# Performance work log

Hardware: AMD Instinct MI355X
Metric: run time of the kernel (lower is better)

The kernel has to match this reference:

```python
import jax, jax.numpy as jnp
import numpy as np

N_FLUID = 16384
N_BND = 2048
SUPPORT = float(np.sqrt(16.0 / (np.pi * N_FLUID)))  # ~16 neighbors avg
NB = 8  # basis functions per axis (n = m = 8)
NM = NB * NB
LAYERS = [32, 64, 64, 2]
F_IN = 8
B_IN = 8


def _radius(queries, points, r):
    """numpy brute-force (chunked) radius search; rows = query idx, cols = point idx."""
    r2 = np.float32(r * r)
    pn = (points ** 2).sum(-1)
    qi_all, pj_all = [], []
    for s in range(0, queries.shape[0], 4096):
        q = queries[s:s + 4096]
        d2 = (q ** 2).sum(-1)[:, None] + pn[None, :] - 2.0 * (q @ points.T)
        qi, pj = np.nonzero(d2 < r2)
        qi_all.append(qi + s)
        pj_all.append(pj)
    return (np.concatenate(qi_all).astype(np.int32),
            np.concatenate(pj_all).astype(np.int32))


def setup_inputs() -> dict:
    rng = np.random.default_rng(0)
    fluid_pos = rng.random((N_FLUID, 2)).astype(np.float32)
    # boundary particles along the perimeter of the unit square
    t = np.linspace(0.0, 4.0, N_BND, endpoint=False).astype(np.float32)
    side = np.floor(t).astype(np.int64)
    frac = t - side
    bx = np.where(side == 0, frac, np.where(side == 1, 1.0, np.where(side == 2, 1.0 - frac, 0.0)))
    by = np.where(side == 0, 0.0, np.where(side == 1, frac, np.where(side == 2, 1.0, 1.0 - frac)))
    bnd_pos = np.stack([bx, by], -1).astype(np.float32)

    # fluid-fluid radius graph (centerIgnore: drop self edges)
    fi, fj = _radius(fluid_pos, fluid_pos, SUPPORT)
    keep = fi != fj
    f_tgt, f_src = fi[keep], fj[keep]
    # fluid(query) - boundary(source) radius graph
    b_tgt, b_src = _radius(fluid_pos, bnd_pos, SUPPORT)

    def conv_w(k, cin, cout):
        return (0.05 * rng.standard_normal((NM, cin, cout))).astype(np.float32)

    def lin_w(cin, cout):
        s = np.sqrt(6.0 / (cin + cout))
        return rng.uniform(-s, s, (cin, cout)).astype(np.float32)

    d = {
        'fluid_pos': jnp.asarray(fluid_pos),
        'bnd_pos': jnp.asarray(bnd_pos),
        'fluid_feat': jnp.asarray(rng.standard_normal((N_FLUID, F_IN)).astype(np.float32)),
        'bnd_feat': jnp.asarray(rng.standard_normal((N_BND, B_IN)).astype(np.float32)),
        'f_tgt': jnp.asarray(f_tgt), 'f_src': jnp.asarray(f_src),
        'b_tgt': jnp.asarray(b_tgt), 'b_src': jnp.asarray(b_src),
        # convs: c0 fluid->fluid (F_IN->32), c1 boundary->fluid (B_IN->32),
        #        c2 (96->64), c3 (64->64), c4 (64->2)
        'Wc0': jnp.asarray(conv_w(0, F_IN, 32)), 'bc0': jnp.zeros((32,), jnp.float32),
        'Wc1': jnp.asarray(conv_w(1, B_IN, 32)), 'bc1': jnp.zeros((32,), jnp.float32),
        'Wc2': jnp.asarray(conv_w(2, 96, 64)), 'bc2': jnp.zeros((64,), jnp.float32),
        'Wc3': jnp.asarray(conv_w(3, 64, 64)), 'bc3': jnp.zeros((64,), jnp.float32),
        'Wc4': jnp.asarray(conv_w(4, 64, 2)), 'bc4': jnp.zeros((2,), jnp.float32),
        # dense branch: l0 (F_IN->32), l1 (96->64), l2 (64->64), l3 (64->2)
        'Wl0': jnp.asarray(lin_w(F_IN, 32)), 'bl0': jnp.zeros((32,), jnp.float32),
        'Wl1': jnp.asarray(lin_w(96, 64)), 'bl1': jnp.zeros((64,), jnp.float32),
        'Wl2': jnp.asarray(lin_w(64, 64)), 'bl2': jnp.zeros((64,), jnp.float32),
        'Wl3': jnp.asarray(lin_w(64, 2)), 'bl3': jnp.zeros((2,), jnp.float32),
    }
    return d


def _hat(x, n):
    # linear 'hat' RBF basis on centers in [-1, 1]
    c = jnp.linspace(-1.0, 1.0, n, dtype=x.dtype)
    return jnp.maximum(0.0, 1.0 - jnp.abs(x[:, None] - c[None, :]) * ((n - 1) / 2.0))


def _polar(d):
    # polar coordinate mapping of normalized displacement d in [-1,1]^2
    r = jnp.sqrt(jnp.sum(d * d, -1) + 1e-12)
    theta = jnp.arctan2(d[:, 1], d[:, 0])
    return jnp.clip(jnp.stack([2.0 * r - 1.0, theta / jnp.pi], -1), -1.0, 1.0)


def _rbf_conv(x_src_nodes, src, tgt, disp, W, b, num_tgt):
    m = _polar(disp)                                   # [E,2]
    bx = _hat(m[:, 0], NB)                             # [E,n]
    by = _hat(m[:, 1], NB)                             # [E,m]
    basis = (bx[:, :, None] * by[:, None, :]).reshape(-1, NM)  # [E,nm]
    xs = x_src_nodes[src]                              # [E,cin]
    acc0 = jnp.zeros((xs.shape[0], W.shape[-1]), xs.dtype)

    def body(acc, wb):
        Wk, bk = wb
        return acc + bk[:, None] * (xs @ Wk), None

    msg, _ = jax.lax.scan(body, acc0, (W, basis.T))    # sum_k basis_k * (xs @ W_k)
    return jax.ops.segment_sum(msg, tgt, num_segments=num_tgt) + b


def reference(fluid_pos, bnd_pos, fluid_feat, bnd_feat, f_tgt, f_src, b_tgt, b_src,
              Wc0, bc0, Wc1, bc1, Wc2, bc2, Wc3, bc3, Wc4, bc4,
              Wl0, bl0, Wl1, bl1, Wl2, bl2, Wl3, bl3):
    N = fluid_feat.shape[0]
    fdisp = jnp.clip(-(fluid_pos[f_src] - fluid_pos[f_tgt]) / SUPPORT, -1.0, 1.0)
    bdisp = jnp.clip((bnd_pos[b_src] - fluid_pos[b_tgt]) / SUPPORT, -1.0, 1.0)

    lin = fluid_feat @ Wl0 + bl0
    fconv = _rbf_conv(fluid_feat, f_src, f_tgt, fdisp, Wc0, bc0, N)
    bconv = _rbf_conv(bnd_feat, b_src, b_tgt, bdisp, Wc1, bc1, N)
    ans = jnp.concatenate([lin, fconv, bconv], axis=-1)  # [N, 96]

    blocks = [(Wc2, bc2, Wl1, bl1, False), (Wc3, bc3, Wl2, bl2, True), (Wc4, bc4, Wl3, bl3, False)]
    for Wc, bc, Wl, bl, residual in blocks:
        a = jax.nn.relu(ans)
        c = _rbf_conv(a, f_src, f_tgt, fdisp, Wc, bc, N)
        dns = a @ Wl + bl
        ans = c + dns + ans if residual else c + dns
    return ans / 128.0
```

## Files before the change

### kernel.cpp

```cpp
#include <hip/hip_runtime.h>
#include <math.h>
#include <stdint.h>

#define NFL   16384
#define NCC   55
#define PADQ  256

struct EdgeData { int src; int ixiy; float fx; float fy; };

typedef _Float16 half8 __attribute__((ext_vector_type(8)));
typedef __attribute__((ext_vector_type(4))) float f32x4;

__device__ __forceinline__ float frelu(float x){ return x > 0.f ? x : 0.f; }
__device__ __forceinline__ unsigned short f2bf(float f){
    unsigned int u = __float_as_uint(f);
    unsigned int r = (u + 0x7FFFu + ((u >> 16) & 1u)) >> 16;
    return (unsigned short)r;
}

__device__ __forceinline__ EdgeData make_edge(const float* qpos, const float* ppos,
                                              int t, int s, float support, float sgn)
{
    float dx = sgn * (ppos[2*s]   - qpos[2*t])   / support;
    float dy = sgn * (ppos[2*s+1] - qpos[2*t+1]) / support;
    dx = fminf(1.f, fmaxf(-1.f, dx));
    dy = fminf(1.f, fmaxf(-1.f, dy));
    float r  = sqrtf(dx*dx + dy*dy + 1e-12f);
    float th = atan2f(dy, dx);
    float m0 = fminf(1.f, fmaxf(-1.f, 2.f*r - 1.f));
    float m1 = fminf(1.f, fmaxf(-1.f, th * 0.3183098861837907f));
    float u = (m0 + 1.f) * 3.5f;
    float v = (m1 + 1.f) * 3.5f;
    int ix = (int)u; if (ix > 6) ix = 6;
    int iy = (int)v; if (iy > 6) iy = 6;
    EdgeData ed;
    ed.src  = s;
    ed.ixiy = ix*8 + iy;
    ed.fx   = u - (float)ix;
    ed.fy   = v - (float)iy;
    return ed;
}

__global__ __launch_bounds__(256)
void setup_k(const float* __restrict__ fluid_pos, const float* __restrict__ bnd_pos,
             const int* __restrict__ f_tgt, const int* __restrict__ f_src, int nEf,
             const int* __restrict__ b_tgt, const int* __restrict__ b_src, int nEb,
             float support,
             EdgeData* __restrict__ edF, EdgeData* __restrict__ edB,
             int* __restrict__ cnt,
             int* __restrict__ rowptrF, int* __restrict__ rowptrB,
             const float* __restrict__ Wc2, const float* __restrict__ Wc3,
             const float* __restrict__ Wc0,
             _Float16* __restrict__ wt2, _Float16* __restrict__ wt3,
             unsigned short* __restrict__ wb0,
             int nA, int nB, int nC)
{
    __shared__ int lc[64];
    __shared__ _Float16 T[64][98];
    int b = blockIdx.x, tid = threadIdx.x;
    if (b < nA){
        if (tid < 64) lc[tid] = 0;
        __syncthreads();
        int e = b*256 + tid;
        if (e < nEf){
            EdgeData d = make_edge(fluid_pos, fluid_pos, f_tgt[e], f_src[e], support, -1.f);
            edF[e] = d;
            atomicAdd(&lc[d.ixiy], 1);
        }
        __syncthreads();
        if (tid < 64 && lc[tid] > 0) atomicAdd(&cnt[tid], lc[tid]);
    } else if (b < nA + nB){
        int e = (b - nA)*256 + tid;
        if (e < nEb)
            edB[e] = make_edge(fluid_pos, bnd_pos, b_tgt[e], b_src[e], support, 1.f);
    } else if (b < nA + nB + nC){
        int t = (b - nA - nB)*256 + tid;
        if (t > NFL) return;
        if (t == NFL){ rowptrF[NFL] = nEf; return; }
        int lo = 0, hi = nEf;
        while (lo < hi){ int mid = (lo + hi) >> 1; if (f_tgt[mid] < t) lo = mid + 1; else hi = mid; }
        rowptrF[t] = lo;
    } else if (b < nA + nB + 2*nC){
        int t = (b - nA - nB - nC)*256 + tid;
        if (t > NFL) return;
        if (t == NFL){ rowptrB[NFL] = nEb; return; }
        int lo = 0, hi = nEb;
        while (lo < hi){ int mid = (lo + hi) >> 1; if (b_tgt[mid] < t) lo = mid + 1; else hi = mid; }
        rowptrB[t] = lo;
    } else {
        int wb = b - (nA + nB + 2*nC);
        if (wb < 64){
            const float* s = Wc2 + (size_t)wb * 96 * 64;
            for (int i = tid; i < 96*64; i += 256){ int k = i/64, c = i - k*64; T[c][k] = (_Float16)s[i]; }
            __syncthreads();
            _Float16* d = wt2 + (size_t)wb * 64 * 96;
            for (int i = tid; i < 96*64; i += 256){ int c = i/96, k = i - c*96; d[i] = T[c][k]; }
        } else if (wb < 128){
            int cell = wb - 64;
            const float* s = Wc3 + (size_t)cell * 64 * 64;
            for (int i = tid; i < 64*64; i += 256){ int k = i/64, c = i - k*64; T[c][k] = (_Float16)s[i]; }
            __syncthreads();
            _Float16* d = wt3 + (size_t)cell * 64 * 64;
            for (int i = tid; i < 64*64; i += 256){ int c = i/64, k = i - c*64; d[i] = T[c][k]; }
        } else {
            for (int i = tid; i < 64*8*32; i += 256) wb0[i] = f2bf(Wc0[i]);
        }
    }
}

__global__ __launch_bounds__(256)
void scan_pad_k(const int* __restrict__ cnt, int* __restrict__ cellOff,
                int* __restrict__ gcursor, int4* __restrict__ entries)
{
    __shared__ int offS[NCC+1], cntS[NCC];
    int tid = threadIdx.x;
    if (tid < 64) gcursor[tid] = 0;
    if (tid == 0){
        int s = 0;
        for (int k = 0; k < NCC; ++k){
            offS[k] = s; int c = cnt[k]; cntS[k] = c;
            s += ((c + PADQ - 1) / PADQ) * PADQ;
        }
        offS[NCC] = s;
        for (int k = 0; k <= NCC; ++k) cellOff[k] = offS[k];
    }
    __syncthreads();
    for (int k = 0; k < NCC; ++k){
        int base = offS[k] + cntS[k];
        int pads = (offS[k+1] - offS[k]) - cntS[k];
        for (int i = tid; i < pads; i += 256)
            entries[base + i] = make_int4(0, -1, 0, 0);
    }
}

__global__ void scatter_k(const EdgeData* __restrict__ ed, int nE,
                          const int* __restrict__ cellOff,
                          int* __restrict__ gcursor,
                          int4* __restrict__ entries)
{
    __shared__ int lc[64], base[64];
    int tid = threadIdx.x;
    if (tid < 64) lc[tid] = 0;
    __syncthreads();
    int e = blockIdx.x * blockDim.x + tid;
    bool ok = e < nE;
    EdgeData d; int k = 0, r = 0;
    if (ok){ d = ed[e]; k = d.ixiy; r = atomicAdd(&lc[k], 1); }
    __syncthreads();
    if (tid < 64 && lc[tid] > 0) base[tid] = atomicAdd(&gcursor[tid], lc[tid]);
    __syncthreads();
    if (ok){
        int slot = cellOff[k] + base[k] + r;
        entries[slot] = make_int4(d.src, e, __float_as_int(d.fx), __float_as_int(d.fy));
    }
}

template<int CIN>
__global__ __launch_bounds__(256)
void conv_mfma_k(const _Float16* __restrict__ xh,
                 const int4* __restrict__ entries,
                 const int* __restrict__ cellOff,
                 const _Float16* __restrict__ wt,
                 _Float16* __restrict__ msg)
{
    constexpr int COUT = 64;
    constexpr int XROW = CIN*2 + 16;
    constexpr int C16  = CIN*2/16;
    constexpr int NK   = CIN/32;

    __shared__ unsigned char XL[64 * XROW];
    __shared__ float BW[4][64];
    __shared__ int   SRC[64];
    __shared__ int   EID[64];

    int total = cellOff[NCC];
    int pb = blockIdx.x * 256;
    if (pb >= total) return;
    int tid = threadIdx.x;

    int lo_ = 0, hi_ = NCC;
    while (hi_ - lo_ > 1){ int mid = (lo_ + hi_) >> 1; if (cellOff[mid] <= pb) lo_ = mid; else hi_ = mid; }
    const int cell = lo_;
    const int kc[4] = { cell, cell+1, cell+8, cell+9 };

    const int lane = tid & 63, wv = tid >> 6;
    const int lr = lane & 15, lg = lane >> 4;
    const int cb = wv * 16;
    const _Float16* wbase = wt + (size_t)(cb + lr) * CIN + lg * 8;

    half8 bfr[4][NK];
#pragma unroll
    for (int cr = 0; cr < 4; ++cr)
#pragma unroll
        for (int kk = 0; kk < NK; ++kk)
            bfr[cr][kk] = *(const half8*)(wbase + (size_t)kc[cr]*(COUT*CIN) + kk*32);

    for (int ch = 0; ch < 4; ++ch){
        int p0 = pb + ch * 64;

        if (tid < 64){
            int4 en = entries[p0 + tid];
            bool ok = en.y >= 0;
            float fx = __int_as_float(en.z), fy = __int_as_float(en.w);
            BW[0][tid] = ok ? (1.f-fx)*(1.f-fy) : 0.f;
            BW[1][tid] = ok ? (1.f-fx)*fy       : 0.f;
            BW[2][tid] = ok ? fx*(1.f-fy)       : 0.f;
            BW[3][tid] = ok ? fx*fy             : 0.f;
            SRC[tid] = en.x;
            EID[tid] = en.y;
        }
        __syncthreads();
        for (int i = tid; i < 64*C16; i += 256){
            int e = i / C16, c = i - e*C16;
            const uint4* sp = (const uint4*)(xh + (size_t)SRC[e]*CIN) + c;
            *(uint4*)(&XL[e*XROW + 16*c]) = *sp;
        }
        __syncthreads();

        f32x4 acc[4][4];
#pragma unroll
        for (int cr = 0; cr < 4; ++cr)
#pragma unroll
            for (int ae = 0; ae < 4; ++ae)
                acc[cr][ae] = (f32x4)0.f;

#pragma unroll
        for (int kk = 0; kk < NK; ++kk){
            half8 a[4];
#pragma unroll
            for (int ae = 0; ae < 4; ++ae)
                a[ae] = *(const half8*)(XL + (16*ae + lr)*XROW + kk*64 + lg*16);
#pragma unroll
            for (int cr = 0; cr < 4; ++cr)
#pragma unroll
                for (int ae = 0; ae < 4; ++ae)
                    acc[cr][ae] = __builtin_amdgcn_mfma_f32_16x16x32_f16(a[ae], bfr[cr][kk], acc[cr][ae], 0, 0, 0);
        }

#pragma unroll
        for (int ae = 0; ae < 4; ++ae){
#pragma unroll
            for (int r = 0; r < 4; ++r){
                int E = 16*ae + lg*4 + r;
                int eid = EID[E];
                if (eid >= 0){
                    float v = BW[0][E]*acc[0][ae][r] + BW[1][E]*acc[1][ae][r]
                            + BW[2][E]*acc[2][ae][r] + BW[3][E]*acc[3][ae][r];
                    msg[(size_t)eid*COUT + cb + lr] = (_Float16)v;
                }
            }
        }
        __syncthreads();
    }
}

template<int CIN, int COUT, int TILE_E, bool RELU>
__global__ __launch_bounds__(128)
void conv_cell_k(const float* __restrict__ x,
                 const int4* __restrict__ entries,
                 const int* __restrict__ cellOff,
                 const unsigned short* __restrict__ Wbf,
                 _Float16* __restrict__ msg)
{
    constexpr int TEP = TILE_E + 4;
    constexpr int EG  = TILE_E / 4;
    constexpr int CG  = COUT / 8;
    static_assert(EG * CG == 128, "tile/thread mismatch");
    constexpr int C4  = CIN / 4;

    __shared__ float XT[CIN][TEP];
    __shared__ unsigned short WLc[4][CIN][COUT];
    __shared__ int4 EN[TILE_E];

    int total = cellOff[NCC];
    int p0 = blockIdx.x * TILE_E;
    if (p0 >= total) return;
    int tid = threadIdx.x;

    int lo = 0, hi = NCC;
    while (hi - lo > 1){ int mid = (lo + hi) >> 1; if (cellOff[mid] <= p0) lo = mid; else hi = mid; }
    const int cell = lo;

    for (int i = tid; i < TILE_E; i += 128) EN[i] = entries[p0 + i];

    const int kc[4] = { cell, cell + 1, cell + 8, cell + 9 };
#pragma unroll
    for (int c = 0; c < 4; ++c){
        const uint4* s = (const uint4*)(Wbf + (size_t)kc[c] * (CIN * COUT));
        uint4* dlds = (uint4*)(&WLc[c][0][0]);
        for (int i = tid; i < CIN * COUT / 8; i += 128) dlds[i] = s[i];
    }
    __syncthreads();

    for (int i = tid; i < TILE_E * C4; i += 128){
        int e  = i / C4;
        int c4 = i - e * C4;
        int4 en = EN[e];
        float4 v = make_float4(0.f, 0.f, 0.f, 0.f);
        if (en.y >= 0){
            v = *(const float4*)(x + (size_t)en.x * CIN + 4 * c4);
            if (RELU){ v.x = frelu(v.x); v.y = frelu(v.y); v.z = frelu(v.z); v.w = frelu(v.w); }
        }
        XT[4*c4+0][e] = v.x;
        XT[4*c4+1][e] = v.y;
        XT[4*c4+2][e] = v.z;
        XT[4*c4+3][e] = v.w;
    }
    __syncthreads();

    const int egrp = tid % EG;
    const int cgrp = tid / EG;
    const int e0 = egrp * 4;

    float fx[4], fy[4];
    int eid[4];
#pragma unroll
    for (int j = 0; j < 4; ++j){
        int4 en = EN[e0 + j];
        fx[j] = __int_as_float(en.z);
        fy[j] = __int_as_float(en.w);
        eid[j] = en.y;
    }

    float accT[4][8];
#pragma unroll
    for (int j = 0; j < 4; ++j)
#pragma unroll
        for (int c = 0; c < 8; ++c) accT[j][c] = 0.f;

#pragma unroll
    for (int cr = 0; cr < 4; ++cr){
        float accC[4][8];
#pragma unroll
        for (int j = 0; j < 4; ++j)
#pragma unroll
            for (int c = 0; c < 8; ++c) accC[j][c] = 0.f;

#pragma unroll
        for (int ci = 0; ci < CIN; ++ci){
            float4 xv = *(const float4*)&XT[ci][e0];
            uint4 wp = *(const uint4*)&WLc[cr][ci][cgrp * 8];
            float wf0 = __uint_as_float(wp.x << 16);
            float wf1 = __uint_as_float(wp.x & 0xFFFF0000u);
            float wf2 = __uint_as_float(wp.y << 16);
            float wf3 = __uint_as_float(wp.y & 0xFFFF0000u);
            float wf4 = __uint_as_float(wp.z << 16);
            float wf5 = __uint_as_float(wp.z & 0xFFFF0000u);
            float wf6 = __uint_as_float(wp.w << 16);
            float wf7 = __uint_as_float(wp.w & 0xFFFF0000u);
            const float xe[4] = { xv.x, xv.y, xv.z, xv.w };
#pragma unroll
            for (int j = 0; j < 4; ++j){
                accC[j][0] += xe[j] * wf0;
                accC[j][1] += xe[j] * wf1;
                accC[j][2] += xe[j] * wf2;
                accC[j][3] += xe[j] * wf3;
                accC[j][4] += xe[j] * wf4;
                accC[j][5] += xe[j] * wf5;
                accC[j][6] += xe[j] * wf6;
                accC[j][7] += xe[j] * wf7;
            }
        }
#pragma unroll
        for (int j = 0; j < 4; ++j){
            float wc = (cr == 0) ? (1.f - fx[j]) * (1.f - fy[j]) :
                       (cr == 1) ? (1.f - fx[j]) * fy[j] :
                       (cr == 2) ? fx[j] * (1.f - fy[j]) :
                                   fx[j] * fy[j];
#pragma unroll
            for (int c = 0; c < 8; ++c) accT[j][c] += wc * accC[j][c];
        }
    }

#pragma unroll
    for (int j = 0; j < 4; ++j){
        if (eid[j] < 0) continue;
        half8 hv;
#pragma unroll
        for (int c = 0; c < 8; ++c) hv[c] = (_Float16)accT[j][c];
        *(half8*)(msg + (size_t)eid[j] * COUT + cgrp * 8) = hv;
    }
}

__global__ __launch_bounds__(128)
void conv2_msg_k(const _Float16* __restrict__ xh,
                 const int4* __restrict__ entries,
                 const int* __restrict__ cellOff,
                 const float* __restrict__ Wc,
                 float* __restrict__ msg2)
{
    __shared__ float WLf[4][64][2];
    int total = cellOff[NCC];
    int p0 = blockIdx.x * 128;
    if (p0 >= total) return;
    int tid = threadIdx.x;

    int lo = 0, hi = NCC;
    while (hi - lo > 1){ int mid = (lo + hi) >> 1; if (cellOff[mid] <= p0) lo = mid; else hi = mid; }
    const int cell = lo;
    const int kc[4] = { cell, cell + 1, cell + 8, cell + 9 };
#pragma unroll
    for (int c = 0; c < 4; ++c)
        ((float*)&WLf[c][0][0])[tid] = Wc[(size_t)kc[c] * 128 + tid];
    __syncthreads();

    int4 en = entries[p0 + tid];
    if (en.y < 0) return;
    float fx = __int_as_float(en.z), fy = __int_as_float(en.w);
    const _Float16* xp = xh + (size_t)en.x * 64;

    float a[4][2] = {{0.f,0.f},{0.f,0.f},{0.f,0.f},{0.f,0.f}};
#pragma unroll
    for (int ci = 0; ci < 64; ci += 8){
        half8 v = *(const half8*)(xp + ci);
#pragma unroll
        for (int j = 0; j < 8; ++j){
            float xe = (float)v[j];
#pragma unroll
            for (int cr = 0; cr < 4; ++cr){
                a[cr][0] += xe * WLf[cr][ci+j][0];
                a[cr][1] += xe * WLf[cr][ci+j][1];
            }
        }
    }
    float w0 = (1.f-fx)*(1.f-fy), w1 = (1.f-fx)*fy, w2 = fx*(1.f-fy), w3 = fx*fy;
    float m0 = w0*a[0][0] + w1*a[1][0] + w2*a[2][0] + w3*a[3][0];
    float m1 = w0*a[0][1] + w1*a[1][1] + w2*a[2][1] + w3*a[3][1];
    *(float2*)(msg2 + (size_t)en.y * 2) = make_float2(m0, m1);
}

__global__ __launch_bounds__(256)
void final_combine_k(const _Float16* __restrict__ xh,
                     const float* __restrict__ Wl3, const float* __restrict__ bl3,
                     const float* __restrict__ bc4,
                     const float* __restrict__ msg2,
                     const int* __restrict__ rowptr,
                     float* __restrict__ out)
{
    __shared__ float WS[128];
    int tid = threadIdx.x;
    if (tid < 128) WS[tid] = Wl3[tid];
    __syncthreads();

    int t = blockIdx.x * blockDim.x + tid;
    if (t >= NFL) return;
    int eb = rowptr[t], ee = rowptr[t+1];

    float a0 = bc4[0] + bl3[0];
    float a1 = bc4[1] + bl3[1];
    const _Float16* pr = xh + (size_t)t * 64;
#pragma unroll
    for (int ci = 0; ci < 64; ci += 8){
        half8 v = *(const half8*)(pr + ci);
#pragma unroll
        for (int j = 0; j < 8; ++j){
            float xe = (float)v[j];
            a0 += xe * WS[(ci+j)*2];
            a1 += xe * WS[(ci+j)*2 + 1];
        }
    }
    for (int e = eb; e < ee; ++e){
        float2 m = *(const float2*)(msg2 + (size_t)e * 2);
        a0 += m.x; a1 += m.y;
    }
    out[(size_t)t*2]     = a0 * (1.0f/128.0f);
    out[(size_t)t*2 + 1] = a1 * (1.0f/128.0f);
}

__global__ __launch_bounds__(256)
void combine0_k(const float* __restrict__ feat,
                const float* __restrict__ bnd_feat,
                const float* __restrict__ Wl0, const float* __restrict__ bl0,
                const float* __restrict__ bc0,
                const float* __restrict__ Wc1, const float* __restrict__ bc1,
                const EdgeData* __restrict__ edB,
                const int* __restrict__ rowptrB,
                const _Float16* __restrict__ msg,
                const int* __restrict__ rowptrF,
                float* __restrict__ ansA,
                _Float16* __restrict__ xbA)
{
    int t = blockIdx.x * (blockDim.x >> 6) + (threadIdx.x >> 6);
    if (t >= NFL) return;
    int lane = threadIdx.x & 63;

    if (lane < 32){
        float a = bl0[lane];
#pragma unroll
        for (int ci = 0; ci < 8; ++ci)
            a += feat[t*8 + ci] * Wl0[ci*32 + lane];
        ansA[(size_t)t*96 + lane] = a;
        xbA[(size_t)t*96 + lane]  = (_Float16)frelu(a);

        float b = bc1[lane];
        int eb = rowptrB[t], ee = rowptrB[t+1];
        for (int e = eb; e < ee; ++e){
            EdgeData d = edB[e];
            const float* xp = bnd_feat + (size_t)d.src * 8;
            const float* wp = Wc1 + (size_t)d.ixiy * 256 + lane;
            float t00 = 0.f, t01 = 0.f, t10 = 0.f, t11 = 0.f;
#pragma unroll
            for (int ci = 0; ci < 8; ++ci){
                float xv = xp[ci];
                t00 += xv * wp[ci*32];
                t01 += xv * wp[ci*32 + 256];
                t10 += xv * wp[ci*32 + 2048];
                t11 += xv * wp[ci*32 + 2304];
            }
            float wx1 = d.fx, wy1 = d.fy;
            float wx0 = 1.f - wx1, wy0 = 1.f - wy1;
            b += (wx0*wy0)*t00 + (wx0*wy1)*t01 + (wx1*wy0)*t10 + (wx1*wy1)*t11;
        }
        ansA[(size_t)t*96 + 64 + lane] = b;
        xbA[(size_t)t*96 + 64 + lane]  = (_Float16)frelu(b);
    } else {
        int c = lane - 32;
        float a = bc0[c];
        int eb = rowptrF[t], ee = rowptrF[t+1];
        for (int e = eb; e < ee; ++e)
            a += (float)msg[(size_t)e*32 + c];
        ansA[(size_t)t*96 + 32 + c] = a;
        xbA[(size_t)t*96 + 32 + c]  = (_Float16)frelu(a);
    }
}

template<int CIN, bool RESID, bool WRITE_XB>
__global__ __launch_bounds__(256)
void combine12_k(const float* __restrict__ yprev,
                 const _Float16* __restrict__ xprev,
                 const float* __restrict__ Wl, const float* __restrict__ bl,
                 const float* __restrict__ bc,
                 const _Float16* __restrict__ msg,
                 const int* __restrict__ rowptr,
                 float* __restrict__ y,
                 _Float16* __restrict__ xbnext)
{
    int t = blockIdx.x * (blockDim.x >> 6) + (threadIdx.x >> 6);
    if (t >= NFL) return;
    int lane = threadIdx.x & 63;
    int eb = rowptr[t], ee = rowptr[t+1];

    const _Float16* pr = xprev + (size_t)t * CIN;
    float acc = bc[lane] + bl[lane];
#pragma unroll 8
    for (int ci = 0; ci < CIN; ++ci)
        acc += (float)pr[ci] * Wl[ci*64 + lane];
    if (RESID) acc += yprev[(size_t)t*64 + lane];

    for (int e = eb; e < ee; ++e)
        acc += (float)msg[(size_t)e*64 + lane];
    y[(size_t)t*64 + lane] = acc;

    if (WRITE_XB)
        xbnext[(size_t)t*64 + lane] = (_Float16)frelu(acc);
}

extern "C" void kernel_launch(void* const* d_in, const int* in_sizes, int n_in,
                              void* d_out, int out_size, void* d_ws, size_t ws_size,
                              hipStream_t stream)
{
    const float* fluid_pos  = (const float*)d_in[0];
    const float* bnd_pos    = (const float*)d_in[1];
    const float* fluid_feat = (const float*)d_in[2];
    const float* bnd_feat   = (const float*)d_in[3];
    const int*   f_tgt      = (const int*)  d_in[4];
    const int*   f_src      = (const int*)  d_in[5];
    const int*   b_tgt      = (const int*)  d_in[6];
    const int*   b_src      = (const int*)  d_in[7];
    const float* Wc0 = (const float*)d_in[8];  const float* bc0 = (const float*)d_in[9];
    const float* Wc1 = (const float*)d_in[10]; const float* bc1 = (const float*)d_in[11];
    const float* Wc2 = (const float*)d_in[12]; const float* bc2 = (const float*)d_in[13];
    const float* Wc3 = (const float*)d_in[14]; const float* bc3 = (const float*)d_in[15];
    const float* Wc4 = (const float*)d_in[16]; const float* bc4 = (const float*)d_in[17];
    const float* Wl0 = (const float*)d_in[18]; const float* bl0 = (const float*)d_in[19];
    const float* Wl1 = (const float*)d_in[20]; const float* bl1 = (const float*)d_in[21];
    const float* Wl2 = (const float*)d_in[22]; const float* bl2 = (const float*)d_in[23];
    const float* Wl3 = (const float*)d_in[24]; const float* bl3 = (const float*)d_in[25];

    int nEf = in_sizes[4];
    int nEb = in_sizes[6];
    int entPadMax = nEf + NCC * PADQ;
    float support = (float)sqrt(16.0 / (M_PI * 16384.0));

    char* w = (char*)d_ws;
    auto alloc = [&](size_t bytes){ char* r = w; w += (bytes + 255) & ~(size_t)255; return r; };
    EdgeData* edF      = (EdgeData*)alloc((size_t)nEf * sizeof(EdgeData));
    EdgeData* edB      = (EdgeData*)alloc((size_t)nEb * sizeof(EdgeData));
    int*      cnt      = (int*)     alloc(64 * sizeof(int));
    int*      cellOff  = (int*)     alloc(64 * sizeof(int));
    int*      gcursor  = (int*)     alloc(64 * sizeof(int));
    int*      rowptrF  = (int*)     alloc((NFL+1) * sizeof(int));
    int*      rowptrB  = (int*)     alloc((NFL+1) * sizeof(int));
    int4*     entries  = (int4*)    alloc((size_t)entPadMax * sizeof(int4));
    unsigned short* wb0 = (unsigned short*)alloc((size_t)64*8*32 * 2);
    _Float16* wt2      = (_Float16*)alloc((size_t)64*64*96 * 2);
    _Float16* wt3      = (_Float16*)alloc((size_t)64*64*64 * 2);
    _Float16* xbA      = (_Float16*)alloc((size_t)NFL*96 * 2);
    _Float16* xb1      = (_Float16*)alloc((size_t)NFL*64 * 2);
    _Float16* xb2      = (_Float16*)alloc((size_t)NFL*64 * 2);
    float*    ansA     = (float*)   alloc((size_t)NFL * 96 * sizeof(float));
    float*    y1       = (float*)   alloc((size_t)NFL * 64 * sizeof(float));
    float*    y2       = (float*)   alloc((size_t)NFL * 64 * sizeof(float));
    _Float16* msg      = (_Float16*)alloc((size_t)nEf * 64 * 2);
    float*    msg2     = (float*)   alloc((size_t)nEf * 2 * sizeof(float));

    hipMemsetAsync(cnt, 0, 64 * sizeof(int), stream);
    int nA = (nEf + 255)/256, nB = (nEb + 255)/256, nC = (NFL + 256)/256;
    setup_k<<<nA + nB + 2*nC + 129, 256, 0, stream>>>(fluid_pos, bnd_pos,
                                                      f_tgt, f_src, nEf,
                                                      b_tgt, b_src, nEb, support,
                                                      edF, edB, cnt, rowptrF, rowptrB,
                                                      Wc2, Wc3, Wc0, wt2, wt3, wb0,
                                                      nA, nB, nC);
    scan_pad_k<<<1, 256, 0, stream>>>(cnt, cellOff, gcursor, entries);
    scatter_k<<<nA, 256, 0, stream>>>(edF, nEf, cellOff, gcursor, entries);

    int gridM = (entPadMax + 255) / 256;
    int gridC = (entPadMax + 127) / 128;
    dim3 tgrid(NFL/4);

    conv_cell_k<8,32,128,false><<<gridC, 128, 0, stream>>>(fluid_feat, entries, cellOff, wb0, msg);
    combine0_k<<<tgrid, 256, 0, stream>>>(fluid_feat, bnd_feat, Wl0, bl0, bc0,
                                          Wc1, bc1, edB, rowptrB,
                                          msg, rowptrF, ansA, xbA);

    conv_mfma_k<96><<<gridM, 256, 0, stream>>>(xbA, entries, cellOff, wt2, msg);
    combine12_k<96,false,true><<<tgrid, 256, 0, stream>>>(nullptr, xbA, Wl1, bl1, bc2, msg, rowptrF, y1, xb1);

    conv_mfma_k<64><<<gridM, 256, 0, stream>>>(xb1, entries, cellOff, wt3, msg);
    combine12_k<64,true,true><<<tgrid, 256, 0, stream>>>(y1, xb1, Wl2, bl2, bc3, msg, rowptrF, y2, xb2);

    conv2_msg_k<<<gridC, 128, 0, stream>>>(xb2, entries, cellOff, Wc4, msg2);
    final_combine_k<<<(NFL+255)/256, 256, 0, stream>>>(xb2, Wl3, bl3, bc4, msg2, rowptrF, (float*)d_out);
}
```

Baseline: 284.9 us.

## Load MFMA A-operands straight from global memory and shrink blocks to 64 edges

The MFMA conv kernel no longer stages gathered source rows and bilinear weights in LDS across four 64-edge chunks with barriers. Each block now handles a single 64-edge chunk, each lane loads its entry and A-fragment directly from global memory, and the edge metadata is broadcast with wave shuffles when computing the epilogue. Cell padding drops from 256 to 128 so blocks of 64 stay within one cell. This removes LDS traffic and syncs and adds parallelism, but the per-block weight fragment loads are repeated four times as often and the global A-loads are less coalesced.

```diff
diff --git a/kernel.cpp b/kernel.cpp
--- a/kernel.cpp
+++ b/kernel.cpp
@@ -4,7 +4,7 @@
 
 #define NFL   16384
 #define NCC   55
-#define PADQ  256
+#define PADQ  128
 
 struct EdgeData { int src; int ixiy; float fx; float fy; };
 
@@ -164,30 +164,32 @@
                  _Float16* __restrict__ msg)
 {
     constexpr int COUT = 64;
-    constexpr int XROW = CIN*2 + 16;
-    constexpr int C16  = CIN*2/16;
     constexpr int NK   = CIN/32;
 
-    __shared__ unsigned char XL[64 * XROW];
-    __shared__ float BW[4][64];
-    __shared__ int   SRC[64];
-    __shared__ int   EID[64];
-
     int total = cellOff[NCC];
-    int pb = blockIdx.x * 256;
-    if (pb >= total) return;
+    int p0 = blockIdx.x * 64;
+    if (p0 >= total) return;
     int tid = threadIdx.x;
 
     int lo_ = 0, hi_ = NCC;
-    while (hi_ - lo_ > 1){ int mid = (lo_ + hi_) >> 1; if (cellOff[mid] <= pb) lo_ = mid; else hi_ = mid; }
+    while (hi_ - lo_ > 1){ int mid = (lo_ + hi_) >> 1; if (cellOff[mid] <= p0) lo_ = mid; else hi_ = mid; }
     const int cell = lo_;
     const int kc[4] = { cell, cell+1, cell+8, cell+9 };
 
     const int lane = tid & 63, wv = tid >> 6;
     const int lr = lane & 15, lg = lane >> 4;
     const int cb = wv * 16;
+
+    int srcA[4], eidA[4];
+    float fxA[4], fyA[4];
+#pragma unroll
+    for (int ae = 0; ae < 4; ++ae){
+        int4 en = entries[p0 + 16*ae + lr];
+        srcA[ae] = en.x; eidA[ae] = en.y;
+        fxA[ae] = __int_as_float(en.z); fyA[ae] = __int_as_float(en.w);
+    }
+
     const _Float16* wbase = wt + (size_t)(cb + lr) * CIN + lg * 8;
-
     half8 bfr[4][NK];
 #pragma unroll
     for (int cr = 0; cr < 4; ++cr)
@@ -195,62 +197,42 @@
         for (int kk = 0; kk < NK; ++kk)
             bfr[cr][kk] = *(const half8*)(wbase + (size_t)kc[cr]*(COUT*CIN) + kk*32);
 
-    for (int ch = 0; ch < 4; ++ch){
-        int p0 = pb + ch * 64;
-
-        if (tid < 64){
-            int4 en = entries[p0 + tid];
-            bool ok = en.y >= 0;
-            float fx = __int_as_float(en.z), fy = __int_as_float(en.w);
-            BW[0][tid] = ok ? (1.f-fx)*(1.f-fy) : 0.f;
-            BW[1][tid] = ok ? (1.f-fx)*fy       : 0.f;
-            BW[2][tid] = ok ? fx*(1.f-fy)       : 0.f;
-            BW[3][tid] = ok ? fx*fy             : 0.f;
-            SRC[tid] = en.x;
-            EID[tid] = en.y;
-        }
-        __syncthreads();
-        for (int i = tid; i < 64*C16; i += 256){
-            int e = i / C16, c = i - e*C16;
-            const uint4* sp = (const uint4*)(xh + (size_t)SRC[e]*CIN) + c;
-            *(uint4*)(&XL[e*XROW + 16*c]) = *sp;
-        }
-        __syncthreads();
-
-        f32x4 acc[4][4];
+    f32x4 acc[4][4];
+#pragma unroll
+    for (int cr = 0; cr < 4; ++cr)
+#pragma unroll
+        for (int ae = 0; ae < 4; ++ae)
+            acc[cr][ae] = (f32x4)0.f;
+
+#pragma unroll
+    for (int kk = 0; kk < NK; ++kk){
+        half8 a[4];
+#pragma unroll
+        for (int ae = 0; ae < 4; ++ae)
+            a[ae] = *(const half8*)(xh + (size_t)srcA[ae]*CIN + kk*32 + lg*8);
 #pragma unroll
         for (int cr = 0; cr < 4; ++cr)
 #pragma unroll
             for (int ae = 0; ae < 4; ++ae)
-                acc[cr][ae] = (f32x4)0.f;
-
-#pragma unroll
-        for (int kk = 0; kk < NK; ++kk){
-            half8 a[4];
-#pragma unroll
-            for (int ae = 0; ae < 4; ++ae)
-                a[ae] = *(const half8*)(XL + (16*ae + lr)*XROW + kk*64 + lg*16);
-#pragma unroll
-            for (int cr = 0; cr < 4; ++cr)
-#pragma unroll
-                for (int ae = 0; ae < 4; ++ae)
-                    acc[cr][ae] = __builtin_amdgcn_mfma_f32_16x16x32_f16(a[ae], bfr[cr][kk], acc[cr][ae], 0, 0, 0);
-        }
-
-#pragma unroll
-        for (int ae = 0; ae < 4; ++ae){
-#pragma unroll
-            for (int r = 0; r < 4; ++r){
-                int E = 16*ae + lg*4 + r;
-                int eid = EID[E];
-                if (eid >= 0){
-                    float v = BW[0][E]*acc[0][ae][r] + BW[1][E]*acc[1][ae][r]
-                            + BW[2][E]*acc[2][ae][r] + BW[3][E]*acc[3][ae][r];
-                    msg[(size_t)eid*COUT + cb + lr] = (_Float16)v;
-                }
+                acc[cr][ae] = __builtin_amdgcn_mfma_f32_16x16x32_f16(a[ae], bfr[cr][kk], acc[cr][ae], 0, 0, 0);
+    }
+
+#pragma unroll
+    for (int ae = 0; ae < 4; ++ae){
+#pragma unroll
+        for (int r = 0; r < 4; ++r){
+            int sl  = lg*4 + r;
+            int eid = __shfl(eidA[ae], sl);
+            float fx = __shfl(fxA[ae], sl);
+            float fy = __shfl(fyA[ae], sl);
+            if (eid >= 0){
+                float w00 = (1.f-fx)*(1.f-fy), w01 = (1.f-fx)*fy;
+                float w10 = fx*(1.f-fy),       w11 = fx*fy;
+                float v = w00*acc[0][ae][r] + w01*acc[1][ae][r]
+                        + w10*acc[2][ae][r] + w11*acc[3][ae][r];
+                msg[(size_t)eid*COUT + cb + lr] = (_Float16)v;
             }
         }
-        __syncthreads();
     }
 }
 
@@ -615,7 +597,7 @@
     scan_pad_k<<<1, 256, 0, stream>>>(cnt, cellOff, gcursor, entries);
     scatter_k<<<nA, 256, 0, stream>>>(edF, nEf, cellOff, gcursor, entries);
 
-    int gridM = (entPadMax + 255) / 256;
+    int gridM = (entPadMax + 63) / 64;
     int gridC = (entPadMax + 127) / 128;
     dim3 tgrid(NFL/4);
 
```

Result: slower. 300.9 us (+5.6%).

## Double-buffer gathered features in conv_mfma_k and prefetch next chunk into registers

Applied to the files above, without the earlier changes.

The MFMA conv kernel now keeps two LDS buffers for the gathered source features and edge weights. It prefetches the next chunk's source rows into registers while the current chunk is being computed. Edge metadata and source indices for all four chunks are loaded up front, and one of the two barriers per chunk is removed. The aim is to hide the latency of the irregular gather behind the MFMA work, at the cost of more LDS and more registers.

```diff
diff --git a/kernel.cpp b/kernel.cpp
--- a/kernel.cpp
+++ b/kernel.cpp
@@ -167,11 +167,12 @@
     constexpr int XROW = CIN*2 + 16;
     constexpr int C16  = CIN*2/16;
     constexpr int NK   = CIN/32;
-
-    __shared__ unsigned char XL[64 * XROW];
-    __shared__ float BW[4][64];
-    __shared__ int   SRC[64];
-    __shared__ int   EID[64];
+    constexpr int LPT  = (64*C16)/256;
+    constexpr int NCH  = 4;
+
+    __shared__ unsigned char XL[2][64 * XROW];
+    __shared__ float BW[2][4][64];
+    __shared__ int   EID[2][64];
 
     int total = cellOff[NCC];
     int pb = blockIdx.x * 256;
@@ -186,8 +187,8 @@
     const int lane = tid & 63, wv = tid >> 6;
     const int lr = lane & 15, lg = lane >> 4;
     const int cb = wv * 16;
+
     const _Float16* wbase = wt + (size_t)(cb + lr) * CIN + lg * 8;
-
     half8 bfr[4][NK];
 #pragma unroll
     for (int cr = 0; cr < 4; ++cr)
@@ -195,25 +196,50 @@
         for (int kk = 0; kk < NK; ++kk)
             bfr[cr][kk] = *(const half8*)(wbase + (size_t)kc[cr]*(COUT*CIN) + kk*32);
 
-    for (int ch = 0; ch < 4; ++ch){
-        int p0 = pb + ch * 64;
-
+    int srow[LPT], scol[LPT];
+#pragma unroll
+    for (int j = 0; j < LPT; ++j){
+        int f = tid + j*256;
+        srow[j] = f / C16;
+        scol[j] = f - srow[j]*C16;
+    }
+
+    int4 emeta[NCH];
+#pragma unroll
+    for (int ch = 0; ch < NCH; ++ch)
+        if (tid < 64) emeta[ch] = entries[pb + ch*64 + tid];
+
+    int ssrc[NCH][LPT];
+#pragma unroll
+    for (int ch = 0; ch < NCH; ++ch)
+#pragma unroll
+        for (int j = 0; j < LPT; ++j)
+            ssrc[ch][j] = entries[pb + ch*64 + srow[j]].x;
+
+    uint4 xr[LPT];
+#pragma unroll
+    for (int j = 0; j < LPT; ++j)
+        xr[j] = *((const uint4*)(xh + (size_t)ssrc[0][j]*CIN) + scol[j]);
+
+    for (int ch = 0; ch < NCH; ++ch){
+        int b = ch & 1;
         if (tid < 64){
-            int4 en = entries[p0 + tid];
+            int4 en = emeta[ch];
             bool ok = en.y >= 0;
             float fx = __int_as_float(en.z), fy = __int_as_float(en.w);
-            BW[0][tid] = ok ? (1.f-fx)*(1.f-fy) : 0.f;
-            BW[1][tid] = ok ? (1.f-fx)*fy       : 0.f;
-            BW[2][tid] = ok ? fx*(1.f-fy)       : 0.f;
-            BW[3][tid] = ok ? fx*fy             : 0.f;
-            SRC[tid] = en.x;
-            EID[tid] = en.y;
-        }
-        __syncthreads();
-        for (int i = tid; i < 64*C16; i += 256){
-            int e = i / C16, c = i - e*C16;
-            const uint4* sp = (const uint4*)(xh + (size_t)SRC[e]*CIN) + c;
-            *(uint4*)(&XL[e*XROW + 16*c]) = *sp;
+            BW[b][0][tid] = ok ? (1.f-fx)*(1.f-fy) : 0.f;
+            BW[b][1][tid] = ok ? (1.f-fx)*fy       : 0.f;
+            BW[b][2][tid] = ok ? fx*(1.f-fy)       : 0.f;
+            BW[b][3][tid] = ok ? fx*fy             : 0.f;
+            EID[b][tid] = en.y;
+        }
+#pragma unroll
+        for (int j = 0; j < LPT; ++j)
+            *(uint4*)(&XL[b][srow[j]*XROW + 16*scol[j]]) = xr[j];
+        if (ch + 1 < NCH){
+#pragma unroll
+            for (int j = 0; j < LPT; ++j)
+                xr[j] = *((const uint4*)(xh + (size_t)ssrc[ch+1][j]*CIN) + scol[j]);
         }
         __syncthreads();
 
@@ -229,7 +255,7 @@
             half8 a[4];
 #pragma unroll
             for (int ae = 0; ae < 4; ++ae)
-                a[ae] = *(const half8*)(XL + (16*ae + lr)*XROW + kk*64 + lg*16);
+                a[ae] = *(const half8*)(&XL[b][(16*ae + lr)*XROW + kk*64 + lg*16]);
 #pragma unroll
             for (int cr = 0; cr < 4; ++cr)
 #pragma unroll
@@ -242,15 +268,14 @@
 #pragma unroll
             for (int r = 0; r < 4; ++r){
                 int E = 16*ae + lg*4 + r;
-                int eid = EID[E];
+                int eid = EID[b][E];
                 if (eid >= 0){
-                    float v = BW[0][E]*acc[0][ae][r] + BW[1][E]*acc[1][ae][r]
-                            + BW[2][E]*acc[2][ae][r] + BW[3][E]*acc[3][ae][r];
+                    float v = BW[b][0][E]*acc[0][ae][r] + BW[b][1][E]*acc[1][ae][r]
+                            + BW[b][2][E]*acc[2][ae][r] + BW[b][3][E]*acc[3][ae][r];
                     msg[(size_t)eid*COUT + cb + lr] = (_Float16)v;
                 }
             }
         }
-        __syncthreads();
     }
 }
 
```

After: 301.6 us. 5.9% more time.
